# Performance work log

Measured on AMD Instinct MI355X. Metric: run time of the kernel, lower is better.

The kernel has to match this reference:

```python
import jax, jax.numpy as jnp
import numpy as np

HIDDEN = 128
STATE = 256
SEQ = 4096
BATCH = 16


def _op(q_i, q_j):
    # Binary operator for the parallel scan of the 2x2 block-diagonal recurrence.
    # m: (..., 4, N) holding [A, B, C, D] blocks; f: (..., 2, N) holding [b1, b2].
    m_i, f_i = q_i
    m_j, f_j = q_j
    iA, iB, iC, iD = m_i[..., 0, :], m_i[..., 1, :], m_i[..., 2, :], m_i[..., 3, :]
    jA, jB, jC, jD = m_j[..., 0, :], m_j[..., 1, :], m_j[..., 2, :], m_j[..., 3, :]
    m_new = jnp.stack([
        jA * iA + jB * iC,
        jA * iB + jB * iD,
        jC * iA + jD * iC,
        jC * iB + jD * iD,
    ], axis=-2)
    b1, b2 = f_i[..., 0, :], f_i[..., 1, :]
    f_new = jnp.stack([jA * b1 + jB * b2, jC * b1 + jD * b2], axis=-2) + f_j
    return m_new, f_new


def _apply_linoss_im(A_diag, B, x, step):
    # x: (L, H); B: (N, H); A_diag, step: (N,)
    Bu = x @ B.T                                    # (L, N)
    s2A = step ** 2 * A_diag
    schur = 1.0 / (1.0 + s2A)
    M11 = 1.0 - s2A * schur
    M12 = -step * A_diag * schur
    M21 = step * schur
    M22 = schur
    L, N = x.shape[0], A_diag.shape[0]
    M = jnp.broadcast_to(jnp.stack([M11, M12, M21, M22]), (L, 4, N))  # (L, 4, N)
    F = jnp.stack([M11 * Bu * step, M21 * Bu * step], axis=1)          # (L, 2, N)
    _, xs = jax.lax.associative_scan(_op, (M, F))
    return xs[:, 1, :]  # second state component y_k, shape (L, N)


def setup_inputs() -> dict:
    key = jax.random.key(0)
    kx, kA, ks, kB, kC, kD = jax.random.split(key, 6)
    x = jax.random.normal(kx, (BATCH, SEQ, HIDDEN), dtype=jnp.float32)
    A_diag = jax.random.uniform(kA, (STATE,), dtype=jnp.float32)
    steps = 0.5 * jax.random.normal(ks, (STATE,), dtype=jnp.float32)
    B = jax.random.normal(kB, (STATE, HIDDEN), dtype=jnp.float32) / np.sqrt(HIDDEN)
    C = jax.random.normal(kC, (HIDDEN, STATE), dtype=jnp.float32) / np.sqrt(STATE)
    D = jax.random.normal(kD, (HIDDEN,), dtype=jnp.float32)
    return {"x": x, "A_diag": A_diag, "steps": steps, "B": B, "C": C, "D": D}


def reference(x, A_diag, steps, B, C, D):
    # Parameter projections used by the mixer (LinOSS-IM, non-damped):
    step = jax.nn.sigmoid(steps)
    A = jax.nn.relu(A_diag)

    def per_seq(xs):
        ys = _apply_linoss_im(A, B, xs, step)   # (L, N)
        return ys @ C.T + D * xs                # (L, H)

    return jax.vmap(per_seq)(x)  # (B, L, H)
```

## Files before the change

### kernel.cpp

```cpp
#include <hip/hip_runtime.h>
#include <hip/hip_bf16.h>

#define BATCHN 16
#define SEQ 4096
#define HIDDEN 128
#define STATE 256
#define MTOT (BATCHN*SEQ)
#define NCHUNK 64
#define LCHUNK 64
#define NTILE (MTOT/64)

typedef __bf16 bf16;
typedef __bf16 bf16x4 __attribute__((ext_vector_type(4)));
typedef __bf16 bf16x8 __attribute__((ext_vector_type(8)));
typedef float f32x4 __attribute__((ext_vector_type(4)));

__device__ __forceinline__ void scan_params(const float* __restrict__ A_diag,
        const float* __restrict__ steps, int n,
        float& m11, float& m12, float& m21, float& m22, float& c1, float& c2) {
    float st = 1.0f / (1.0f + expf(-steps[n]));
    float A  = fmaxf(A_diag[n], 0.0f);
    float s2A = st * st * A;
    float schur = 1.0f / (1.0f + s2A);
    m11 = 1.0f - s2A * schur;
    m12 = -st * A * schur;
    m21 = st * schur;
    m22 = schur;
    c1 = m11 * st;
    c2 = m21 * st;
}

__device__ __forceinline__ bf16x8 load_frag_f32(const float* __restrict__ src) {
    float4 a = *reinterpret_cast<const float4*>(src);
    float4 b = *reinterpret_cast<const float4*>(src + 4);
    bf16x8 r = { (bf16)a.x, (bf16)a.y, (bf16)a.z, (bf16)a.w,
                 (bf16)b.x, (bf16)b.y, (bf16)b.z, (bf16)b.w };
    return r;
}

__global__ __launch_bounds__(256, 3) void k1_gemm_scanA(const float* __restrict__ x,
        const float* __restrict__ A_diag, const float* __restrict__ steps,
        const float* __restrict__ Bm, float* __restrict__ cs,
        bf16* __restrict__ Bu_g) {
    __shared__ bf16 xl[64][136];
    __shared__ bf16 bu[64][264];
    const int tid = threadIdx.x;
    const int bid = blockIdx.x;
    const int m0 = bid * 64;
    const int wid = tid >> 6, lane = tid & 63;
    const int lr = lane & 15, lk = (lane >> 4) * 8;
    const int n0 = wid * 64;
    const int mrow = (lane >> 4) * 4;

    #pragma unroll
    for (int p = 0; p < 8; ++p) {
        int flat = p * 256 + tid;
        int row = flat >> 5, c4 = flat & 31;
        float4 v = *reinterpret_cast<const float4*>(&x[(size_t)(m0 + row) * HIDDEN + c4 * 4]);
        bf16x4 w = { (bf16)v.x, (bf16)v.y, (bf16)v.z, (bf16)v.w };
        *reinterpret_cast<bf16x4*>(&xl[row][c4 * 4]) = w;
    }
    __syncthreads();

    f32x4 acc[4][4];
    #pragma unroll
    for (int i = 0; i < 4; ++i)
        #pragma unroll
        for (int j = 0; j < 4; ++j) acc[i][j] = f32x4{0.f, 0.f, 0.f, 0.f};
    #pragma unroll
    for (int ks = 0; ks < 4; ++ks) {
        int k = ks * 32 + lk;
        bf16x8 a[4], bfr[4];
        #pragma unroll
        for (int mf = 0; mf < 4; ++mf)
            a[mf] = *reinterpret_cast<const bf16x8*>(&xl[mf * 16 + lr][k]);
        #pragma unroll
        for (int nf = 0; nf < 4; ++nf)
            bfr[nf] = load_frag_f32(&Bm[(size_t)(n0 + nf * 16 + lr) * HIDDEN + k]);
        #pragma unroll
        for (int mf = 0; mf < 4; ++mf)
            #pragma unroll
            for (int nf = 0; nf < 4; ++nf)
                acc[mf][nf] = __builtin_amdgcn_mfma_f32_16x16x32_bf16(a[mf], bfr[nf], acc[mf][nf], 0, 0, 0);
    }
    #pragma unroll
    for (int mf = 0; mf < 4; ++mf)
        #pragma unroll
        for (int nf = 0; nf < 4; ++nf)
            #pragma unroll
            for (int r = 0; r < 4; ++r)
                bu[mf * 16 + mrow + r][n0 + nf * 16 + lr] = (bf16)acc[mf][nf][r];

    const int n = tid;
    float m11, m12, m21, m22, c1, c2;
    scan_params(A_diag, steps, n, m11, m12, m21, m22, c1, c2);
    __syncthreads();

    #pragma unroll
    for (int p = 0; p < 8; ++p) {
        int flat = p * 256 + tid;
        int row = flat >> 5, c8 = flat & 31;
        bf16x8 v = *reinterpret_cast<const bf16x8*>(&bu[row][c8 * 8]);
        *reinterpret_cast<bf16x8*>(&Bu_g[((size_t)(m0 + row)) * STATE + c8 * 8]) = v;
    }

    float s1 = 0.f, s2 = 0.f;
    #pragma unroll 8
    for (int t = 0; t < LCHUNK; ++t) {
        float v = (float)bu[t][n];
        float ns1 = fmaf(m11, s1, fmaf(m12, s2, c1 * v));
        float ns2 = fmaf(m21, s1, fmaf(m22, s2, c2 * v));
        s1 = ns1; s2 = ns2;
    }
    size_t base = ((size_t)bid * 2) * STATE + n;
    cs[base] = s1;
    cs[base + STATE] = s2;
}

__global__ __launch_bounds__(256, 4) void k2_scan_gemm(const bf16* __restrict__ Bu_g,
        const float* __restrict__ x, const float* __restrict__ A_diag,
        const float* __restrict__ steps, const float* __restrict__ Cm,
        const float* __restrict__ cs, const float* __restrict__ Dv,
        float* __restrict__ out) {
    __shared__ bf16 bu[64][264];
    float (*ldsF)[132] = reinterpret_cast<float(*)[132]>(&bu[0][0]);
    const int tid = threadIdx.x;
    const int bid = blockIdx.x;
    const int m0 = bid * 64;
    const int wid = tid >> 6, lane = tid & 63;
    const int lr = lane & 15, lk = (lane >> 4) * 8;
    const int h0 = wid * 32;
    const int batch = bid >> 6;
    const int chunk = bid & (NCHUNK - 1);
    const int n = tid;
    const int mrow = (lane >> 4) * 4;

    #pragma unroll
    for (int p = 0; p < 8; ++p) {
        int flat = p * 256 + tid;
        int row = flat >> 5, c8 = flat & 31;
        bf16x8 v = *reinterpret_cast<const bf16x8*>(&Bu_g[((size_t)(m0 + row)) * STATE + c8 * 8]);
        *reinterpret_cast<bf16x8*>(&bu[row][c8 * 8]) = v;
    }

    float m11, m12, m21, m22, c1, c2;
    scan_params(A_diag, steps, n, m11, m12, m21, m22, c1, c2);
    float S1 = 0.f, S2 = 0.f;
    if (chunk > 0) {
        float p11 = m11, p12 = m12, p21 = m21, p22 = m22;
        #pragma unroll
        for (int i = 0; i < 6; ++i) {
            float q11 = p11 * p11 + p12 * p21;
            float q12 = p11 * p12 + p12 * p22;
            float q21 = p21 * p11 + p22 * p21;
            float q22 = p21 * p12 + p22 * p22;
            p11 = q11; p12 = q12; p21 = q21; p22 = q22;
        }
        #pragma unroll 4
        for (int j = 0; j < chunk; ++j) {
            size_t base = ((size_t)(batch * NCHUNK + j) * 2) * STATE + n;
            float q1 = cs[base], q2 = cs[base + STATE];
            float n1 = fmaf(p11, S1, fmaf(p12, S2, q1));
            float n2 = fmaf(p21, S1, fmaf(p22, S2, q2));
            S1 = n1; S2 = n2;
        }
    }
    __syncthreads();

    {
        float s1 = S1, s2 = S2;
        #pragma unroll 8
        for (int t = 0; t < LCHUNK; ++t) {
            float v = (float)bu[t][n];
            float ns1 = fmaf(m11, s1, fmaf(m12, s2, c1 * v));
            float ns2 = fmaf(m21, s1, fmaf(m22, s2, c2 * v));
            s1 = ns1; s2 = ns2;
            bu[t][n] = (bf16)s2;
        }
    }
    __syncthreads();

    f32x4 acc2[4][2];
    #pragma unroll
    for (int i = 0; i < 4; ++i) {
        acc2[i][0] = f32x4{0.f, 0.f, 0.f, 0.f};
        acc2[i][1] = f32x4{0.f, 0.f, 0.f, 0.f};
    }
    #pragma unroll
    for (int ks = 0; ks < 8; ++ks) {
        int k = ks * 32 + lk;
        bf16x8 a[4], cfr[2];
        #pragma unroll
        for (int mf = 0; mf < 4; ++mf)
            a[mf] = *reinterpret_cast<const bf16x8*>(&bu[mf * 16 + lr][k]);
        #pragma unroll
        for (int hf = 0; hf < 2; ++hf)
            cfr[hf] = load_frag_f32(&Cm[(size_t)(h0 + hf * 16 + lr) * STATE + k]);
        #pragma unroll
        for (int mf = 0; mf < 4; ++mf)
            #pragma unroll
            for (int hf = 0; hf < 2; ++hf)
                acc2[mf][hf] = __builtin_amdgcn_mfma_f32_16x16x32_bf16(a[mf], cfr[hf], acc2[mf][hf], 0, 0, 0);
    }
    __syncthreads();
    #pragma unroll
    for (int mf = 0; mf < 4; ++mf)
        #pragma unroll
        for (int hf = 0; hf < 2; ++hf)
            #pragma unroll
            for (int r = 0; r < 4; ++r)
                ldsF[mf * 16 + mrow + r][h0 + hf * 16 + lr] = acc2[mf][hf][r];
    __syncthreads();

    #pragma unroll
    for (int p = 0; p < 8; ++p) {
        int flat = p * 256 + tid;
        int row = flat >> 5, c4 = flat & 31;
        float4 xv = *reinterpret_cast<const float4*>(&x[(size_t)(m0 + row) * HIDDEN + c4 * 4]);
        float4 f = *reinterpret_cast<const float4*>(&ldsF[row][c4 * 4]);
        float4 d = *reinterpret_cast<const float4*>(&Dv[c4 * 4]);
        float4 o;
        o.x = f.x + d.x * xv.x;
        o.y = f.y + d.y * xv.y;
        o.z = f.z + d.z * xv.z;
        o.w = f.w + d.w * xv.w;
        *reinterpret_cast<float4*>(&out[(size_t)(m0 + row) * HIDDEN + c4 * 4]) = o;
    }
}

extern "C" void kernel_launch(void* const* d_in, const int* in_sizes, int n_in,
                              void* d_out, int out_size, void* d_ws, size_t ws_size,
                              hipStream_t stream) {
    const float* x      = (const float*)d_in[0];
    const float* A_diag = (const float*)d_in[1];
    const float* steps  = (const float*)d_in[2];
    const float* Bm     = (const float*)d_in[3];
    const float* Cm     = (const float*)d_in[4];
    const float* Dv     = (const float*)d_in[5];
    float* out = (float*)d_out;

    char* ws = (char*)d_ws;
    const size_t CS_BYTES = (size_t)NTILE * 2 * STATE * 4;
    float* cs   = (float*)ws;
    bf16*  Bu_g = (bf16*)(ws + CS_BYTES);

    hipLaunchKernelGGL(k1_gemm_scanA, dim3(NTILE), dim3(256), 0, stream,
                       x, A_diag, steps, Bm, cs, Bu_g);
    hipLaunchKernelGGL(k2_scan_gemm, dim3(NTILE), dim3(256), 0, stream,
                       Bu_g, x, A_diag, steps, Cm, cs, Dv, out);
}
```

Measured before the change: 63.40 us.

## Add Kogge-Stone chunk-carry scan kernel and alias x tile into bu LDS

A new small kernel turns the per-chunk carry summaries into exclusive prefix carries using a wavefront shuffle-based Kogge-Stone scan over the 64 chunks, applying matrix powers M^64·2^r. Each block of k2 then reads its carry directly, where before it ran a serial loop over all earlier chunks (up to 63 dependent steps). k1 also reuses the bu LDS buffer for the x tile, adding a barrier, so LDS use drops and the launch bound is raised to 4 blocks per CU. The cost is one extra kernel launch and a dependency between three kernels.

```diff
diff --git a/kernel.cpp b/kernel.cpp
--- a/kernel.cpp
+++ b/kernel.cpp
@@ -38,11 +38,10 @@
     return r;
 }
 
-__global__ __launch_bounds__(256, 3) void k1_gemm_scanA(const float* __restrict__ x,
+__global__ __launch_bounds__(256, 4) void k1_gemm_scanA(const float* __restrict__ x,
         const float* __restrict__ A_diag, const float* __restrict__ steps,
         const float* __restrict__ Bm, float* __restrict__ cs,
         bf16* __restrict__ Bu_g) {
-    __shared__ bf16 xl[64][136];
     __shared__ bf16 bu[64][264];
     const int tid = threadIdx.x;
     const int bid = blockIdx.x;
@@ -58,7 +57,7 @@
         int row = flat >> 5, c4 = flat & 31;
         float4 v = *reinterpret_cast<const float4*>(&x[(size_t)(m0 + row) * HIDDEN + c4 * 4]);
         bf16x4 w = { (bf16)v.x, (bf16)v.y, (bf16)v.z, (bf16)v.w };
-        *reinterpret_cast<bf16x4*>(&xl[row][c4 * 4]) = w;
+        *reinterpret_cast<bf16x4*>(&bu[row][c4 * 4]) = w;
     }
     __syncthreads();
 
@@ -73,7 +72,7 @@
         bf16x8 a[4], bfr[4];
         #pragma unroll
         for (int mf = 0; mf < 4; ++mf)
-            a[mf] = *reinterpret_cast<const bf16x8*>(&xl[mf * 16 + lr][k]);
+            a[mf] = *reinterpret_cast<const bf16x8*>(&bu[mf * 16 + lr][k]);
         #pragma unroll
         for (int nf = 0; nf < 4; ++nf)
             bfr[nf] = load_frag_f32(&Bm[(size_t)(n0 + nf * 16 + lr) * HIDDEN + k]);
@@ -83,6 +82,7 @@
             for (int nf = 0; nf < 4; ++nf)
                 acc[mf][nf] = __builtin_amdgcn_mfma_f32_16x16x32_bf16(a[mf], bfr[nf], acc[mf][nf], 0, 0, 0);
     }
+    __syncthreads();
     #pragma unroll
     for (int mf = 0; mf < 4; ++mf)
         #pragma unroll
@@ -115,6 +115,51 @@
     size_t base = ((size_t)bid * 2) * STATE + n;
     cs[base] = s1;
     cs[base + STATE] = s2;
+}
+
+__global__ __launch_bounds__(256) void scan_comb_ks(float* __restrict__ cs,
+        const float* __restrict__ A_diag, const float* __restrict__ steps) {
+    const int c    = threadIdx.x & 63;
+    const int nsub = threadIdx.x >> 6;
+    const int b    = blockIdx.x >> 2;
+    const int nb   = blockIdx.x & 3;
+    #pragma nounroll
+    for (int i = 0; i < 16; ++i) {
+        const int n = nb * 64 + i * 4 + nsub;
+        float m11, m12, m21, m22, cu1, cu2;
+        scan_params(A_diag, steps, n, m11, m12, m21, m22, cu1, cu2);
+        float p11 = m11, p12 = m12, p21 = m21, p22 = m22;
+        #pragma unroll
+        for (int r = 0; r < 6; ++r) {
+            float q11 = p11 * p11 + p12 * p21;
+            float q12 = p11 * p12 + p12 * p22;
+            float q21 = p21 * p11 + p22 * p21;
+            float q22 = p21 * p12 + p22 * p22;
+            p11 = q11; p12 = q12; p21 = q21; p22 = q22;
+        }
+        size_t base = ((size_t)(b * NCHUNK + c) * 2) * STATE + n;
+        float V1 = cs[base], V2 = cs[base + STATE];
+        #pragma unroll
+        for (int r = 0; r < 6; ++r) {
+            int d = 1 << r;
+            float U1 = __shfl_up(V1, d, 64);
+            float U2 = __shfl_up(V2, d, 64);
+            if (c >= d) {
+                V1 = fmaf(p11, U1, fmaf(p12, U2, V1));
+                V2 = fmaf(p21, U1, fmaf(p22, U2, V2));
+            }
+            float q11 = p11 * p11 + p12 * p21;
+            float q12 = p11 * p12 + p12 * p22;
+            float q21 = p21 * p11 + p22 * p21;
+            float q22 = p21 * p12 + p22 * p22;
+            p11 = q11; p12 = q12; p21 = q21; p22 = q22;
+        }
+        float E1 = __shfl_up(V1, 1, 64);
+        float E2 = __shfl_up(V2, 1, 64);
+        if (c == 0) { E1 = 0.f; E2 = 0.f; }
+        cs[base] = E1;
+        cs[base + STATE] = E2;
+    }
 }
 
 __global__ __launch_bounds__(256, 4) void k2_scan_gemm(const bf16* __restrict__ Bu_g,
@@ -130,8 +175,6 @@
     const int wid = tid >> 6, lane = tid & 63;
     const int lr = lane & 15, lk = (lane >> 4) * 8;
     const int h0 = wid * 32;
-    const int batch = bid >> 6;
-    const int chunk = bid & (NCHUNK - 1);
     const int n = tid;
     const int mrow = (lane >> 4) * 4;
 
@@ -145,38 +188,17 @@
 
     float m11, m12, m21, m22, c1, c2;
     scan_params(A_diag, steps, n, m11, m12, m21, m22, c1, c2);
-    float S1 = 0.f, S2 = 0.f;
-    if (chunk > 0) {
-        float p11 = m11, p12 = m12, p21 = m21, p22 = m22;
-        #pragma unroll
-        for (int i = 0; i < 6; ++i) {
-            float q11 = p11 * p11 + p12 * p21;
-            float q12 = p11 * p12 + p12 * p22;
-            float q21 = p21 * p11 + p22 * p21;
-            float q22 = p21 * p12 + p22 * p22;
-            p11 = q11; p12 = q12; p21 = q21; p22 = q22;
-        }
-        #pragma unroll 4
-        for (int j = 0; j < chunk; ++j) {
-            size_t base = ((size_t)(batch * NCHUNK + j) * 2) * STATE + n;
-            float q1 = cs[base], q2 = cs[base + STATE];
-            float n1 = fmaf(p11, S1, fmaf(p12, S2, q1));
-            float n2 = fmaf(p21, S1, fmaf(p22, S2, q2));
-            S1 = n1; S2 = n2;
-        }
-    }
-    __syncthreads();
-
-    {
-        float s1 = S1, s2 = S2;
-        #pragma unroll 8
-        for (int t = 0; t < LCHUNK; ++t) {
-            float v = (float)bu[t][n];
-            float ns1 = fmaf(m11, s1, fmaf(m12, s2, c1 * v));
-            float ns2 = fmaf(m21, s1, fmaf(m22, s2, c2 * v));
-            s1 = ns1; s2 = ns2;
-            bu[t][n] = (bf16)s2;
-        }
+    size_t cbase = ((size_t)bid * 2) * STATE + n;
+    float s1 = cs[cbase], s2 = cs[cbase + STATE];
+    __syncthreads();
+
+    #pragma unroll 8
+    for (int t = 0; t < LCHUNK; ++t) {
+        float v = (float)bu[t][n];
+        float ns1 = fmaf(m11, s1, fmaf(m12, s2, c1 * v));
+        float ns2 = fmaf(m21, s1, fmaf(m22, s2, c2 * v));
+        s1 = ns1; s2 = ns2;
+        bu[t][n] = (bf16)s2;
     }
     __syncthreads();
 
@@ -246,6 +268,8 @@
 
     hipLaunchKernelGGL(k1_gemm_scanA, dim3(NTILE), dim3(256), 0, stream,
                        x, A_diag, steps, Bm, cs, Bu_g);
+    hipLaunchKernelGGL(scan_comb_ks, dim3(BATCHN * 4), dim3(256), 0, stream,
+                       cs, A_diag, steps);
     hipLaunchKernelGGL(k2_scan_gemm, dim3(NTILE), dim3(256), 0, stream,
                        Bu_g, x, A_diag, steps, Cm, cs, Dv, out);
 }
```

After: 73.71 us. 16.3% more time.
